# Kernel tuning notes

Measured on AMD Instinct MI355X. Metric: run time of the kernel, lower is better.

The kernel has to match this reference:

```python
import jax, jax.numpy as jnp
import numpy as np

B, S, E = 2, 2048, 1024
H, KV, D = 16, 4, 64
GC = 128          # ve_gate_channels
EPS = 1.1920929e-07  # torch F.rms_norm default eps for fp32
NEG = -1e30


def setup_inputs() -> dict:
    key = jax.random.key(0)
    ks = jax.random.split(key, 8)
    x = jax.random.normal(ks[0], (B, S, E), jnp.float32)
    ve = jax.random.normal(ks[1], (B, S, KV * D), jnp.float32)
    half = D // 2
    inv_freq = 1.0 / (10000.0 ** (np.arange(half, dtype=np.float64) / half))
    ang = np.arange(S, dtype=np.float64)[:, None] * inv_freq[None, :]
    cos = jnp.asarray(np.cos(ang), jnp.float32)[:, None, :]  # [S,1,D/2]
    sin = jnp.asarray(np.sin(ang), jnp.float32)[:, None, :]
    sc = E ** -0.5
    Wq = jax.random.normal(ks[2], (E, H * D), jnp.float32) * sc
    Wk = jax.random.normal(ks[3], (E, KV * D), jnp.float32) * sc
    Wv = jax.random.normal(ks[4], (E, KV * D), jnp.float32) * sc
    Wproj = jax.random.normal(ks[5], (E, E), jnp.float32) * sc
    Wgate = jax.random.normal(ks[6], (GC, KV), jnp.float32) * (GC ** -0.5)
    return {"x": x, "ve": ve, "cos": cos, "sin": sin, "Wq": Wq, "Wk": Wk,
            "Wv": Wv, "Wproj": Wproj, "Wgate": Wgate,
            "window_left": 1024, "window_right": 0}


def _rms(x):
    return x * jax.lax.rsqrt(jnp.mean(x * x, axis=-1, keepdims=True) + EPS)


def _rope(x, cos, sin):
    d = x.shape[-1] // 2
    x1, x2 = x[..., :d], x[..., d:]
    return jnp.concatenate([x1 * cos + x2 * sin, -x1 * sin + x2 * cos], axis=-1)


def reference(x, ve, cos, sin, Wq, Wk, Wv, Wproj, Wgate, window_left, window_right):
    b, s, e = x.shape
    q = (x @ Wq).reshape(b, s, H, D)
    k = (x @ Wk).reshape(b, s, KV, D)
    v = (x @ Wv).reshape(b, s, KV, D)
    # value-embedding gate: 2*sigmoid over first GC channels, per kv-head
    gate = 2.0 * jax.nn.sigmoid(x[..., :GC] @ Wgate)          # [B,S,KV]
    v = v + gate[..., None] * ve.reshape(b, s, KV, D)
    q = _rms(_rope(q, cos, sin))
    k = _rms(_rope(k, cos, sin))
    # GQA: repeat kv heads to match query heads
    g = H // KV
    kk = jnp.repeat(k, g, axis=2)                             # [B,S,H,D]
    vv = jnp.repeat(v, g, axis=2)
    scores = jnp.einsum('bihd,bjhd->bhij', q, kk) * (D ** -0.5)
    i = jnp.arange(s)[:, None]
    j = jnp.arange(s)[None, :]
    mask = (j <= i + window_right) & (j >= i - window_left) & (j <= i)
    scores = jnp.where(mask, scores, NEG)
    p = jax.nn.softmax(scores, axis=-1)
    y = jnp.einsum('bhij,bjhd->bihd', p, vv).reshape(b, s, H * D)
    return y @ Wproj
```

## Files before the change

kernel.cpp:

```cpp
#include <hip/hip_runtime.h>

typedef __bf16 bf16;
typedef __bf16 bf16x4 __attribute__((ext_vector_type(4)));
typedef __bf16 bf16x8 __attribute__((ext_vector_type(8)));
typedef float floatx4 __attribute__((ext_vector_type(4)));

#define EPS 1.1920929e-07f
#define QSCALE (0.125f * 1.44269504088896f)
#define SHIFT_C 11.5416f

__device__ __forceinline__ floatx4 mfma16(bf16x8 a, bf16x8 b, floatx4 c) {
  return __builtin_amdgcn_mfma_f32_16x16x32_bf16(a, b, c, 0, 0, 0);
}

__device__ __forceinline__ void gload16(const void* g, void* l) {
  __builtin_amdgcn_global_load_lds((const __attribute__((address_space(1))) unsigned int*)g,
                                   (__attribute__((address_space(3))) unsigned int*)l, 16, 0, 0);
}

__global__ void cast_gate_kernel(const float* __restrict__ x, const float* __restrict__ wgate,
                                 bf16* __restrict__ xb, float* __restrict__ gate) {
  int t = blockIdx.x, tid = threadIdx.x;
  const float* xr = x + (size_t)t * 1024;
  float4 v = *(const float4*)(xr + tid * 4);
  bf16x4 o = {(bf16)v.x, (bf16)v.y, (bf16)v.z, (bf16)v.w};
  *(bf16x4*)(xb + (size_t)t * 1024 + tid * 4) = o;
  if (tid < 64) {
    int c = (tid & 31) * 4;
#pragma unroll
    for (int kv = 0; kv < 4; kv++) {
      float g = v.x * wgate[(c + 0) * 4 + kv] + v.y * wgate[(c + 1) * 4 + kv] +
                v.z * wgate[(c + 2) * 4 + kv] + v.w * wgate[(c + 3) * 4 + kv];
      g += __shfl_xor(g, 1, 64);
      g += __shfl_xor(g, 2, 64);
      g += __shfl_xor(g, 4, 64);
      g += __shfl_xor(g, 8, 64);
      g += __shfl_xor(g, 16, 64);
      if (tid == 0) {
        int b = t >> 11, s = t & 2047;
        gate[((size_t)b * 4 + kv) * 2048 + s] = 2.f / (1.f + __expf(-g));
      }
    }
  }
}

__global__ void pack_w_kernel(const float* __restrict__ Wq, const float* __restrict__ Wk,
                              const float* __restrict__ Wv, const float* __restrict__ Wproj,
                              bf16* __restrict__ out_qkv, bf16* __restrict__ out_proj) {
  __shared__ float tile[32][33];
  int k0 = blockIdx.y * 32;
  int tx = threadIdx.x & 31, ty = threadIdx.x >> 5;
  if (blockIdx.x < 48) {
    int n0 = blockIdx.x * 32;
#pragma unroll
    for (int i = 0; i < 4; i++) {
      int k = k0 + ty + i * 8, n = n0 + tx;
      float v;
      if (n < 1024)      v = Wq[(size_t)k * 1024 + n];
      else if (n < 1280) v = Wk[(size_t)k * 256 + (n - 1024)];
      else               v = Wv[(size_t)k * 256 + (n - 1280)];
      tile[ty + i * 8][tx] = v;
    }
    __syncthreads();
#pragma unroll
    for (int i = 0; i < 4; i++) {
      int n = n0 + ty + i * 8, k = k0 + tx;
      out_qkv[(size_t)n * 1024 + k] = (bf16)tile[tx][ty + i * 8];
    }
  } else {
    int n0 = (blockIdx.x - 48) * 32;
#pragma unroll
    for (int i = 0; i < 4; i++)
      tile[ty + i * 8][tx] = Wproj[(size_t)(k0 + ty + i * 8) * 1024 + n0 + tx];
    __syncthreads();
#pragma unroll
    for (int i = 0; i < 4; i++)
      out_proj[(size_t)(n0 + ty + i * 8) * 1024 + k0 + tx] = (bf16)tile[tx][ty + i * 8];
  }
}

__global__ __launch_bounds__(256) void qkv_gemm_kernel(const bf16* __restrict__ A,
                                                       const bf16* __restrict__ Bt,
                                                       const float* __restrict__ ve,
                                                       const float* __restrict__ cosb,
                                                       const float* __restrict__ sinb,
                                                       const float* __restrict__ gate,
                                                       bf16* __restrict__ Qb,
                                                       bf16* __restrict__ Kf,
                                                       bf16* __restrict__ Vf) {
  __shared__ __align__(16) char smem[24576];
  bf16* As = (bf16*)smem;
  bf16* Bs = (bf16*)(smem + 16384);
  bf16* Ep = (bf16*)smem;
  const int K = 1024;
  const int tid = threadIdx.x;
  const int tile = blockIdx.x;
  const int m0 = blockIdx.y * 128, n0 = tile * 64;
  const int w = tid >> 6, lane = tid & 63;
  const int q = lane >> 4, r0 = lane & 15;
  const int lrow = lane >> 2, lcol = (lane & 3) * 8;
  const int b = m0 >> 11, s0 = m0 & 2047;

  floatx4 acc[2][4];
#pragma unroll
  for (int i = 0; i < 2; i++)
#pragma unroll
    for (int j = 0; j < 4; j++) acc[i][j] = (floatx4){0.f, 0.f, 0.f, 0.f};

  for (int k0 = 0; k0 < K; k0 += 64) {
    __syncthreads();
#pragma unroll
    for (int i = 0; i < 4; i++) {
      int g = w * 4 + i, s = g >> 3, rb = g & 7;
      gload16(A + (size_t)(m0 + rb * 16 + lrow) * K + k0 + s * 32 + lcol, &As[s * 4096 + rb * 512]);
    }
#pragma unroll
    for (int i = 0; i < 2; i++) {
      int g = w * 2 + i, s = g >> 2, rb = g & 3;
      gload16(Bt + (size_t)(n0 + rb * 16 + lrow) * K + k0 + s * 32 + lcol, &Bs[s * 2048 + rb * 512]);
    }
    __syncthreads();
#pragma unroll
    for (int s = 0; s < 2; s++) {
      bf16x8 af[2], bfr[4];
#pragma unroll
      for (int mt = 0; mt < 2; mt++) af[mt] = *(const bf16x8*)&As[s * 4096 + (w * 32 + mt * 16 + r0) * 32 + q * 8];
#pragma unroll
      for (int nt = 0; nt < 4; nt++) bfr[nt] = *(const bf16x8*)&Bs[s * 2048 + (nt * 16 + r0) * 32 + q * 8];
#pragma unroll
      for (int mt = 0; mt < 2; mt++)
#pragma unroll
        for (int nt = 0; nt < 4; nt++)
          acc[mt][nt] = mfma16(af[mt], bfr[nt], acc[mt][nt]);
    }
  }
  __syncthreads();

  if (tile < 16) {
    const int h = tile;
#pragma unroll
    for (int mt = 0; mt < 2; mt++) {
      float rvv[4][4];
#pragma unroll
      for (int ntp = 0; ntp < 2; ntp++) {
        int d31 = ntp * 16 + r0;
#pragma unroll
        for (int r = 0; r < 4; r++) {
          int s = s0 + w * 32 + mt * 16 + q * 4 + r;
          float c = cosb[s * 32 + d31], sn = sinb[s * 32 + d31];
          float v1 = acc[mt][ntp][r], v2 = acc[mt][ntp + 2][r];
          rvv[ntp][r] = v1 * c + v2 * sn;
          rvv[ntp + 2][r] = v2 * c - v1 * sn;
        }
      }
#pragma unroll
      for (int r = 0; r < 4; r++) {
        float ss = 0.f;
#pragma unroll
        for (int nt = 0; nt < 4; nt++) ss += rvv[nt][r] * rvv[nt][r];
        ss += __shfl_xor(ss, 1, 64);
        ss += __shfl_xor(ss, 2, 64);
        ss += __shfl_xor(ss, 4, 64);
        ss += __shfl_xor(ss, 8, 64);
        float sc = rsqrtf(ss * (1.f / 64.f) + EPS) * QSCALE;
        int row = w * 32 + mt * 16 + q * 4 + r;
#pragma unroll
        for (int nt = 0; nt < 4; nt++)
          Ep[row * 72 + nt * 16 + r0] = (bf16)(rvv[nt][r] * sc);
      }
    }
    __syncthreads();
#pragma unroll
    for (int p = 0; p < 4; p++) {
      int g = p * 256 + tid;
      int row = g >> 3, chunk = g & 7;
      *(uint4*)&Qb[(((size_t)b * 16 + h) * 2048 + s0 + row) * 64 + chunk * 8] =
          *(const uint4*)&Ep[row * 72 + chunk * 8];
    }
  } else if (tile < 20) {
    const int kv = tile - 16;
#pragma unroll
    for (int mt = 0; mt < 2; mt++) {
      float rvv[4][4];
#pragma unroll
      for (int ntp = 0; ntp < 2; ntp++) {
        int d31 = ntp * 16 + r0;
#pragma unroll
        for (int r = 0; r < 4; r++) {
          int s = s0 + w * 32 + mt * 16 + q * 4 + r;
          float c = cosb[s * 32 + d31], sn = sinb[s * 32 + d31];
          float v1 = acc[mt][ntp][r], v2 = acc[mt][ntp + 2][r];
          rvv[ntp][r] = v1 * c + v2 * sn;
          rvv[ntp + 2][r] = v2 * c - v1 * sn;
        }
      }
#pragma unroll
      for (int r = 0; r < 4; r++) {
        float ss = 0.f;
#pragma unroll
        for (int nt = 0; nt < 4; nt++) ss += rvv[nt][r] * rvv[nt][r];
        ss += __shfl_xor(ss, 1, 64);
        ss += __shfl_xor(ss, 2, 64);
        ss += __shfl_xor(ss, 4, 64);
        ss += __shfl_xor(ss, 8, 64);
        float sc = rsqrtf(ss * (1.f / 64.f) + EPS);
        int row = w * 32 + mt * 16 + q * 4 + r;
#pragma unroll
        for (int nt = 0; nt < 4; nt++)
          Ep[row * 72 + nt * 16 + r0] = (bf16)(rvv[nt][r] * sc);
      }
    }
    __syncthreads();
    {
      int tk = (s0 >> 5) + w;
      size_t tb = ((size_t)(b * 4 + kv) * 64 + tk) * 2048;
#pragma unroll
      for (int u = 0; u < 4; u++) {
        int joff = (u >= 2) ? 16 : 0, doff = (u & 1) * 32;
        bf16x8 f = *(const bf16x8*)&Ep[(w * 32 + joff + r0) * 72 + doff + q * 8];
        *(bf16x8*)&Kf[tb + u * 512 + lane * 8] = f;
      }
    }
  } else {
    const int kv = tile - 20;
    const float* gbase = gate + ((size_t)b * 4 + kv) * 2048;
#pragma unroll
    for (int mt = 0; mt < 2; mt++) {
#pragma unroll
      for (int r = 0; r < 4; r++) {
        int row = w * 32 + mt * 16 + q * 4 + r;
        float gg = gbase[s0 + row];
#pragma unroll
        for (int nt = 0; nt < 4; nt++) {
          int d = nt * 16 + r0;
          float vv = acc[mt][nt][r] + gg * ve[(size_t)(m0 + row) * 256 + kv * 64 + d];
          Ep[row * 72 + d] = (bf16)vv;
        }
      }
    }
    __syncthreads();
    {
      int tk = (s0 >> 5) + w;
      size_t tb = ((size_t)(b * 4 + kv) * 64 + tk) * 2048;
#pragma unroll
      for (int nt = 0; nt < 4; nt++) {
        bf16 tmp[8];
#pragma unroll
        for (int e = 0; e < 8; e++) {
          int jl = w * 32 + (e >> 2) * 16 + 4 * q + (e & 3);
          tmp[e] = Ep[jl * 72 + nt * 16 + r0];
        }
        *(uint4*)&Vf[tb + nt * 512 + lane * 8] = *(uint4*)tmp;
      }
    }
  }
}

__global__ __launch_bounds__(256) void proj_gemm_kernel(const bf16* __restrict__ A,
                                                        const bf16* __restrict__ Bt,
                                                        float* __restrict__ Cout) {
  __shared__ __align__(16) bf16 As[2 * 128 * 32];
  __shared__ __align__(16) bf16 Bs[2 * 64 * 32];
  const int K = 1024, N = 1024;
  const int tid = threadIdx.x;
  const int m0 = blockIdx.y * 128, n0 = blockIdx.x * 64;
  const int w = tid >> 6, lane = tid & 63;
  const int q = lane >> 4, r0 = lane & 15;
  const int lrow = lane >> 2, lcol = (lane & 3) * 8;

  floatx4 acc[2][4];
#pragma unroll
  for (int i = 0; i < 2; i++)
#pragma unroll
    for (int j = 0; j < 4; j++) acc[i][j] = (floatx4){0.f, 0.f, 0.f, 0.f};

  for (int k0 = 0; k0 < K; k0 += 64) {
    __syncthreads();
#pragma unroll
    for (int i = 0; i < 4; i++) {
      int g = w * 4 + i, s = g >> 3, rb = g & 7;
      gload16(A + (size_t)(m0 + rb * 16 + lrow) * K + k0 + s * 32 + lcol, &As[s * 4096 + rb * 512]);
    }
#pragma unroll
    for (int i = 0; i < 2; i++) {
      int g = w * 2 + i, s = g >> 2, rb = g & 3;
      gload16(Bt + (size_t)(n0 + rb * 16 + lrow) * K + k0 + s * 32 + lcol, &Bs[s * 2048 + rb * 512]);
    }
    __syncthreads();
#pragma unroll
    for (int s = 0; s < 2; s++) {
      bf16x8 af[2], bfr[4];
#pragma unroll
      for (int mt = 0; mt < 2; mt++) af[mt] = *(const bf16x8*)&As[s * 4096 + (w * 32 + mt * 16 + r0) * 32 + q * 8];
#pragma unroll
      for (int nt = 0; nt < 4; nt++) bfr[nt] = *(const bf16x8*)&Bs[s * 2048 + (nt * 16 + r0) * 32 + q * 8];
#pragma unroll
      for (int mt = 0; mt < 2; mt++)
#pragma unroll
        for (int nt = 0; nt < 4; nt++)
          acc[mt][nt] = mfma16(af[mt], bfr[nt], acc[mt][nt]);
    }
  }
#pragma unroll
  for (int mt = 0; mt < 2; mt++)
#pragma unroll
    for (int nt = 0; nt < 4; nt++)
#pragma unroll
      for (int r = 0; r < 4; r++) {
        int row = m0 + w * 32 + mt * 16 + q * 4 + r;
        int col = n0 + nt * 16 + r0;
        Cout[(size_t)row * N + col] = acc[mt][nt][r];
      }
}

__global__ __launch_bounds__(512) void attn_kernel(const bf16* __restrict__ Qb,
                                                   const bf16* __restrict__ Kf,
                                                   const bf16* __restrict__ Vf,
                                                   const int* __restrict__ wlp,
                                                   const int* __restrict__ wrp,
                                                   bf16* __restrict__ Yb) {
  const int wl = wlp[0];
  const int wrc = min(wrp[0], 0);
  const int blk = blockIdx.x;
  const int cpair = blk & 31, bkv = blk >> 5;
  const int b = bkv >> 2, kvh = bkv & 3;
  const int w = threadIdx.x >> 6, lane = threadIdx.x & 63;
  const int q = lane >> 4, r0 = lane & 15;
  const int h = kvh * 4 + (w & 3);
  const int cm = (w < 4) ? cpair : 63 - cpair;
  const int q0 = cm * 32;
  const int qA = q0, qB = q0 + 16;

  const bf16* qbase = Qb + (((size_t)b * 16 + h) * 2048 + qA + r0) * 64;
  bf16x8 aqA0 = *(const bf16x8*)(qbase + q * 8);
  bf16x8 aqA1 = *(const bf16x8*)(qbase + 32 + q * 8);
  bf16x8 aqB0 = *(const bf16x8*)(qbase + 16 * 64 + q * 8);
  bf16x8 aqB1 = *(const bf16x8*)(qbase + 16 * 64 + 32 + q * 8);

  floatx4 OA[4], OB[4];
#pragma unroll
  for (int nt = 0; nt < 4; nt++) {
    OA[nt] = (floatx4){0.f, 0.f, 0.f, 0.f};
    OB[nt] = (floatx4){0.f, 0.f, 0.f, 0.f};
  }
  floatx4 LA = (floatx4){0.f, 0.f, 0.f, 0.f};
  floatx4 LB = LA;

  const bf16 onev = (bf16)1.0f;
  const bf16x8 ones = {onev, onev, onev, onev, onev, onev, onev, onev};

  const int jlo = max(0, q0 - wl) & ~31;
  const int jhi = q0 + 31 + wrc;
  const int count = ((jhi - jlo) >> 5) + 1;
  const int tile0 = jlo >> 5;

  const bf16* kfb = Kf + ((size_t)(b * 4 + kvh) * 64) * 2048 + lane * 8;
  const bf16* vfb = Vf + ((size_t)(b * 4 + kvh) * 64) * 2048 + lane * 8;

  bf16x8 kf[4], vf[4], nk[4], nv[4];
#pragma unroll
  for (int u = 0; u < 4; u++) {
    kf[u] = *(const bf16x8*)(kfb + (size_t)tile0 * 2048 + u * 512);
    vf[u] = *(const bf16x8*)(vfb + (size_t)tile0 * 2048 + u * 512);
  }

  for (int t = 0; t < count; t++) {
    const int j0 = jlo + (t << 5);
    const int tn = (t + 1 < count) ? tile0 + t + 1 : tile0 + t;
#pragma unroll
    for (int u = 0; u < 4; u++) {
      nk[u] = *(const bf16x8*)(kfb + (size_t)tn * 2048 + u * 512);
      nv[u] = *(const bf16x8*)(vfb + (size_t)tn * 2048 + u * 512);
    }

    floatx4 sA0 = (floatx4){-SHIFT_C, -SHIFT_C, -SHIFT_C, -SHIFT_C};
    floatx4 sA1 = sA0, sB0 = sA0, sB1 = sA0;
    sA0 = mfma16(kf[0], aqA0, sA0);
    sA0 = mfma16(kf[1], aqA1, sA0);
    sA1 = mfma16(kf[2], aqA0, sA1);
    sA1 = mfma16(kf[3], aqA1, sA1);
    sB0 = mfma16(kf[0], aqB0, sB0);
    sB0 = mfma16(kf[1], aqB1, sB0);
    sB1 = mfma16(kf[2], aqB0, sB1);
    sB1 = mfma16(kf[3], aqB1, sB1);

    bf16x8 paA, paB;
    if (j0 >= qA + 15 - wl && j0 + 31 <= qA + wrc) {
#pragma unroll
      for (int r = 0; r < 4; r++) {
        paA[r] = (bf16)exp2f(sA0[r]);
        paA[4 + r] = (bf16)exp2f(sA1[r]);
      }
    } else {
      const int i = qA + r0;
#pragma unroll
      for (int r = 0; r < 4; r++) {
        int ja = j0 + 4 * q + r, jb = ja + 16;
        bool va = (ja <= i + wrc) && (ja >= i - wl);
        bool vb = (jb <= i + wrc) && (jb >= i - wl);
        paA[r] = va ? (bf16)exp2f(sA0[r]) : (bf16)0.f;
        paA[4 + r] = vb ? (bf16)exp2f(sA1[r]) : (bf16)0.f;
      }
    }
    if (j0 >= qB + 15 - wl && j0 + 31 <= qB + wrc) {
#pragma unroll
      for (int r = 0; r < 4; r++) {
        paB[r] = (bf16)exp2f(sB0[r]);
        paB[4 + r] = (bf16)exp2f(sB1[r]);
      }
    } else {
      const int i = qB + r0;
#pragma unroll
      for (int r = 0; r < 4; r++) {
        int ja = j0 + 4 * q + r, jb = ja + 16;
        bool va = (ja <= i + wrc) && (ja >= i - wl);
        bool vb = (jb <= i + wrc) && (jb >= i - wl);
        paB[r] = va ? (bf16)exp2f(sB0[r]) : (bf16)0.f;
        paB[4 + r] = vb ? (bf16)exp2f(sB1[r]) : (bf16)0.f;
      }
    }

    LA = mfma16(paA, ones, LA);
    LB = mfma16(paB, ones, LB);
#pragma unroll
    for (int nt = 0; nt < 4; nt++) {
      OA[nt] = mfma16(paA, vf[nt], OA[nt]);
      OB[nt] = mfma16(paB, vf[nt], OB[nt]);
    }

#pragma unroll
    for (int u = 0; u < 4; u++) { kf[u] = nk[u]; vf[u] = nv[u]; }
  }

  float invA[4], invB[4];
#pragma unroll
  for (int r = 0; r < 4; r++) {
    invA[r] = 1.f / LA[r];
    invB[r] = 1.f / LB[r];
  }
#pragma unroll
  for (int nt = 0; nt < 4; nt++)
#pragma unroll
    for (int r = 0; r < 4; r++) {
      int iA = qA + q * 4 + r;
      Yb[((size_t)b * 2048 + iA) * 1024 + h * 64 + nt * 16 + r0] = (bf16)(OA[nt][r] * invA[r]);
      int iB = qB + q * 4 + r;
      Yb[((size_t)b * 2048 + iB) * 1024 + h * 64 + nt * 16 + r0] = (bf16)(OB[nt][r] * invB[r]);
    }
}

extern "C" void kernel_launch(void* const* d_in, const int* in_sizes, int n_in,
                              void* d_out, int out_size, void* d_ws, size_t ws_size,
                              hipStream_t stream) {
  const float* x     = (const float*)d_in[0];
  const float* ve    = (const float*)d_in[1];
  const float* cosb  = (const float*)d_in[2];
  const float* sinb  = (const float*)d_in[3];
  const float* Wq    = (const float*)d_in[4];
  const float* Wk    = (const float*)d_in[5];
  const float* Wv    = (const float*)d_in[6];
  const float* Wproj = (const float*)d_in[7];
  const float* Wgate = (const float*)d_in[8];
  const int* wl      = (const int*)d_in[9];
  const int* wr      = (const int*)d_in[10];

  char* ws = (char*)d_ws;
  bf16* Xb      = (bf16*)(ws);
  bf16* Wqkv_t  = (bf16*)(ws + 8388608);
  bf16* Wproj_t = (bf16*)(ws + 11534336);
  bf16* Qb      = (bf16*)(ws + 13631488);
  bf16* Kf      = (bf16*)(ws + 22020096);
  bf16* Vf      = (bf16*)(ws + 24117248);
  bf16* Yb      = (bf16*)(ws + 26214400);
  float* gateb  = (float*)(ws + 34603008);

  cast_gate_kernel<<<4096, 256, 0, stream>>>(x, Wgate, Xb, gateb);
  pack_w_kernel<<<dim3(80, 32), 256, 0, stream>>>(Wq, Wk, Wv, Wproj, Wqkv_t, Wproj_t);
  qkv_gemm_kernel<<<dim3(24, 32), 256, 0, stream>>>(Xb, Wqkv_t, ve, cosb, sinb, gateb, Qb, Kf, Vf);
  attn_kernel<<<256, 512, 0, stream>>>(Qb, Kf, Vf, wl, wr, Yb);
  proj_gemm_kernel<<<dim3(16, 32), 256, 0, stream>>>(Yb, Wproj_t, (float*)d_out);
}
```

Baseline: 171.4 us.

## Merge prep kernels and split attention into smaller 16-row blocks

Merges the x cast/gate kernel and the weight pack/transpose kernel into one launch, removing one kernel launch and its tail. Restructures attention so each 256-thread block handles one 16-query-row chunk for four heads, launching 1024 blocks ordered heaviest-first instead of 256 blocks that paired mirrored 32-row chunks. It also adds s_setprio around the MFMA groups. This raises the number of blocks and occupancy for load balance, but K/V tiles are now reloaded per 16 query rows instead of shared across two 16-row halves, which increases K/V memory traffic.

```diff
diff --git a/kernel.cpp b/kernel.cpp
--- a/kernel.cpp
+++ b/kernel.cpp
@@ -18,64 +18,69 @@
                                    (__attribute__((address_space(3))) unsigned int*)l, 16, 0, 0);
 }
 
-__global__ void cast_gate_kernel(const float* __restrict__ x, const float* __restrict__ wgate,
-                                 bf16* __restrict__ xb, float* __restrict__ gate) {
-  int t = blockIdx.x, tid = threadIdx.x;
-  const float* xr = x + (size_t)t * 1024;
-  float4 v = *(const float4*)(xr + tid * 4);
-  bf16x4 o = {(bf16)v.x, (bf16)v.y, (bf16)v.z, (bf16)v.w};
-  *(bf16x4*)(xb + (size_t)t * 1024 + tid * 4) = o;
-  if (tid < 64) {
-    int c = (tid & 31) * 4;
-#pragma unroll
-    for (int kv = 0; kv < 4; kv++) {
-      float g = v.x * wgate[(c + 0) * 4 + kv] + v.y * wgate[(c + 1) * 4 + kv] +
-                v.z * wgate[(c + 2) * 4 + kv] + v.w * wgate[(c + 3) * 4 + kv];
-      g += __shfl_xor(g, 1, 64);
-      g += __shfl_xor(g, 2, 64);
-      g += __shfl_xor(g, 4, 64);
-      g += __shfl_xor(g, 8, 64);
-      g += __shfl_xor(g, 16, 64);
-      if (tid == 0) {
-        int b = t >> 11, s = t & 2047;
-        gate[((size_t)b * 4 + kv) * 2048 + s] = 2.f / (1.f + __expf(-g));
-      }
-    }
-  }
-}
-
-__global__ void pack_w_kernel(const float* __restrict__ Wq, const float* __restrict__ Wk,
-                              const float* __restrict__ Wv, const float* __restrict__ Wproj,
-                              bf16* __restrict__ out_qkv, bf16* __restrict__ out_proj) {
+__global__ void prep_kernel(const float* __restrict__ x, const float* __restrict__ wgate,
+                            const float* __restrict__ Wq, const float* __restrict__ Wk,
+                            const float* __restrict__ Wv, const float* __restrict__ Wproj,
+                            bf16* __restrict__ xb, float* __restrict__ gate,
+                            bf16* __restrict__ out_qkv, bf16* __restrict__ out_proj) {
   __shared__ float tile[32][33];
-  int k0 = blockIdx.y * 32;
-  int tx = threadIdx.x & 31, ty = threadIdx.x >> 5;
-  if (blockIdx.x < 48) {
-    int n0 = blockIdx.x * 32;
-#pragma unroll
-    for (int i = 0; i < 4; i++) {
-      int k = k0 + ty + i * 8, n = n0 + tx;
-      float v;
-      if (n < 1024)      v = Wq[(size_t)k * 1024 + n];
-      else if (n < 1280) v = Wk[(size_t)k * 256 + (n - 1024)];
-      else               v = Wv[(size_t)k * 256 + (n - 1280)];
-      tile[ty + i * 8][tx] = v;
-    }
-    __syncthreads();
-#pragma unroll
-    for (int i = 0; i < 4; i++) {
-      int n = n0 + ty + i * 8, k = k0 + tx;
-      out_qkv[(size_t)n * 1024 + k] = (bf16)tile[tx][ty + i * 8];
+  const int tid = threadIdx.x;
+  if (blockIdx.x < 4096) {
+    int t = blockIdx.x;
+    const float* xr = x + (size_t)t * 1024;
+    float4 v = *(const float4*)(xr + tid * 4);
+    bf16x4 o = {(bf16)v.x, (bf16)v.y, (bf16)v.z, (bf16)v.w};
+    *(bf16x4*)(xb + (size_t)t * 1024 + tid * 4) = o;
+    if (tid < 64) {
+      int c = (tid & 31) * 4;
+#pragma unroll
+      for (int kv = 0; kv < 4; kv++) {
+        float g = v.x * wgate[(c + 0) * 4 + kv] + v.y * wgate[(c + 1) * 4 + kv] +
+                  v.z * wgate[(c + 2) * 4 + kv] + v.w * wgate[(c + 3) * 4 + kv];
+        g += __shfl_xor(g, 1, 64);
+        g += __shfl_xor(g, 2, 64);
+        g += __shfl_xor(g, 4, 64);
+        g += __shfl_xor(g, 8, 64);
+        g += __shfl_xor(g, 16, 64);
+        if (tid == 0) {
+          int b = t >> 11, s = t & 2047;
+          gate[((size_t)b * 4 + kv) * 2048 + s] = 2.f / (1.f + __expf(-g));
+        }
+      }
     }
   } else {
-    int n0 = (blockIdx.x - 48) * 32;
-#pragma unroll
-    for (int i = 0; i < 4; i++)
-      tile[ty + i * 8][tx] = Wproj[(size_t)(k0 + ty + i * 8) * 1024 + n0 + tx];
-    __syncthreads();
-#pragma unroll
-    for (int i = 0; i < 4; i++)
-      out_proj[(size_t)(n0 + ty + i * 8) * 1024 + k0 + tx] = (bf16)tile[tx][ty + i * 8];
+    int j = blockIdx.x - 4096;
+    int ky = j / 80;
+    int nx = j - ky * 80;
+    int k0 = ky * 32;
+    int tx = tid & 31, ty = tid >> 5;
+    if (nx < 48) {
+      int n0 = nx * 32;
+#pragma unroll
+      for (int i = 0; i < 4; i++) {
+        int k = k0 + ty + i * 8, n = n0 + tx;
+        float v;
+        if (n < 1024)      v = Wq[(size_t)k * 1024 + n];
+        else if (n < 1280) v = Wk[(size_t)k * 256 + (n - 1024)];
+        else               v = Wv[(size_t)k * 256 + (n - 1280)];
+        tile[ty + i * 8][tx] = v;
+      }
+      __syncthreads();
+#pragma unroll
+      for (int i = 0; i < 4; i++) {
+        int n = n0 + ty + i * 8, k = k0 + tx;
+        out_qkv[(size_t)n * 1024 + k] = (bf16)tile[tx][ty + i * 8];
+      }
+    } else {
+      int n0 = (nx - 48) * 32;
+#pragma unroll
+      for (int i = 0; i < 4; i++)
+        tile[ty + i * 8][tx] = Wproj[(size_t)(k0 + ty + i * 8) * 1024 + n0 + tx];
+      __syncthreads();
+#pragma unroll
+      for (int i = 0; i < 4; i++)
+        out_proj[(size_t)(n0 + ty + i * 8) * 1024 + k0 + tx] = (bf16)tile[tx][ty + i * 8];
+    }
   }
 }
 
@@ -313,44 +318,37 @@
       }
 }
 
-__global__ __launch_bounds__(512) void attn_kernel(const bf16* __restrict__ Qb,
-                                                   const bf16* __restrict__ Kf,
-                                                   const bf16* __restrict__ Vf,
-                                                   const int* __restrict__ wlp,
-                                                   const int* __restrict__ wrp,
-                                                   bf16* __restrict__ Yb) {
+__global__ __launch_bounds__(256, 4) void attn_kernel(const bf16* __restrict__ Qb,
+                                                      const bf16* __restrict__ Kf,
+                                                      const bf16* __restrict__ Vf,
+                                                      const int* __restrict__ wlp,
+                                                      const int* __restrict__ wrp,
+                                                      bf16* __restrict__ Yb) {
   const int wl = wlp[0];
   const int wrc = min(wrp[0], 0);
   const int blk = blockIdx.x;
-  const int cpair = blk & 31, bkv = blk >> 5;
+  const int bkv = blk & 7;
   const int b = bkv >> 2, kvh = bkv & 3;
+  const int cm = 127 - (blk >> 3);
   const int w = threadIdx.x >> 6, lane = threadIdx.x & 63;
   const int q = lane >> 4, r0 = lane & 15;
-  const int h = kvh * 4 + (w & 3);
-  const int cm = (w < 4) ? cpair : 63 - cpair;
-  const int q0 = cm * 32;
-  const int qA = q0, qB = q0 + 16;
-
-  const bf16* qbase = Qb + (((size_t)b * 16 + h) * 2048 + qA + r0) * 64;
-  bf16x8 aqA0 = *(const bf16x8*)(qbase + q * 8);
-  bf16x8 aqA1 = *(const bf16x8*)(qbase + 32 + q * 8);
-  bf16x8 aqB0 = *(const bf16x8*)(qbase + 16 * 64 + q * 8);
-  bf16x8 aqB1 = *(const bf16x8*)(qbase + 16 * 64 + 32 + q * 8);
-
-  floatx4 OA[4], OB[4];
-#pragma unroll
-  for (int nt = 0; nt < 4; nt++) {
-    OA[nt] = (floatx4){0.f, 0.f, 0.f, 0.f};
-    OB[nt] = (floatx4){0.f, 0.f, 0.f, 0.f};
-  }
-  floatx4 LA = (floatx4){0.f, 0.f, 0.f, 0.f};
-  floatx4 LB = LA;
+  const int h = kvh * 4 + w;
+  const int q0 = cm << 4;
+
+  const bf16* qbase = Qb + (((size_t)b * 16 + h) * 2048 + q0 + r0) * 64;
+  bf16x8 aq0 = *(const bf16x8*)(qbase + q * 8);
+  bf16x8 aq1 = *(const bf16x8*)(qbase + 32 + q * 8);
+
+  floatx4 O[4];
+#pragma unroll
+  for (int nt = 0; nt < 4; nt++) O[nt] = (floatx4){0.f, 0.f, 0.f, 0.f};
+  floatx4 L = (floatx4){0.f, 0.f, 0.f, 0.f};
 
   const bf16 onev = (bf16)1.0f;
   const bf16x8 ones = {onev, onev, onev, onev, onev, onev, onev, onev};
 
   const int jlo = max(0, q0 - wl) & ~31;
-  const int jhi = q0 + 31 + wrc;
+  const int jhi = q0 + 15 + wrc;
   const int count = ((jhi - jlo) >> 5) + 1;
   const int tile0 = jlo >> 5;
 
@@ -373,79 +371,53 @@
       nv[u] = *(const bf16x8*)(vfb + (size_t)tn * 2048 + u * 512);
     }
 
-    floatx4 sA0 = (floatx4){-SHIFT_C, -SHIFT_C, -SHIFT_C, -SHIFT_C};
-    floatx4 sA1 = sA0, sB0 = sA0, sB1 = sA0;
-    sA0 = mfma16(kf[0], aqA0, sA0);
-    sA0 = mfma16(kf[1], aqA1, sA0);
-    sA1 = mfma16(kf[2], aqA0, sA1);
-    sA1 = mfma16(kf[3], aqA1, sA1);
-    sB0 = mfma16(kf[0], aqB0, sB0);
-    sB0 = mfma16(kf[1], aqB1, sB0);
-    sB1 = mfma16(kf[2], aqB0, sB1);
-    sB1 = mfma16(kf[3], aqB1, sB1);
-
-    bf16x8 paA, paB;
-    if (j0 >= qA + 15 - wl && j0 + 31 <= qA + wrc) {
-#pragma unroll
-      for (int r = 0; r < 4; r++) {
-        paA[r] = (bf16)exp2f(sA0[r]);
-        paA[4 + r] = (bf16)exp2f(sA1[r]);
+    floatx4 s0 = (floatx4){-SHIFT_C, -SHIFT_C, -SHIFT_C, -SHIFT_C};
+    floatx4 s1 = s0;
+    __builtin_amdgcn_s_setprio(1);
+    s0 = mfma16(kf[0], aq0, s0);
+    s0 = mfma16(kf[1], aq1, s0);
+    s1 = mfma16(kf[2], aq0, s1);
+    s1 = mfma16(kf[3], aq1, s1);
+    __builtin_amdgcn_s_setprio(0);
+
+    bf16x8 pa;
+    if (j0 >= q0 + 15 - wl && j0 + 31 <= q0 + wrc) {
+#pragma unroll
+      for (int r = 0; r < 4; r++) {
+        pa[r] = (bf16)exp2f(s0[r]);
+        pa[4 + r] = (bf16)exp2f(s1[r]);
       }
     } else {
-      const int i = qA + r0;
+      const int i = q0 + r0;
 #pragma unroll
       for (int r = 0; r < 4; r++) {
         int ja = j0 + 4 * q + r, jb = ja + 16;
         bool va = (ja <= i + wrc) && (ja >= i - wl);
         bool vb = (jb <= i + wrc) && (jb >= i - wl);
-        paA[r] = va ? (bf16)exp2f(sA0[r]) : (bf16)0.f;
-        paA[4 + r] = vb ? (bf16)exp2f(sA1[r]) : (bf16)0.f;
-      }
-    }
-    if (j0 >= qB + 15 - wl && j0 + 31 <= qB + wrc) {
-#pragma unroll
-      for (int r = 0; r < 4; r++) {
-        paB[r] = (bf16)exp2f(sB0[r]);
-        paB[4 + r] = (bf16)exp2f(sB1[r]);
-      }
-    } else {
-      const int i = qB + r0;
-#pragma unroll
-      for (int r = 0; r < 4; r++) {
-        int ja = j0 + 4 * q + r, jb = ja + 16;
-        bool va = (ja <= i + wrc) && (ja >= i - wl);
-        bool vb = (jb <= i + wrc) && (jb >= i - wl);
-        paB[r] = va ? (bf16)exp2f(sB0[r]) : (bf16)0.f;
-        paB[4 + r] = vb ? (bf16)exp2f(sB1[r]) : (bf16)0.f;
-      }
-    }
-
-    LA = mfma16(paA, ones, LA);
-    LB = mfma16(paB, ones, LB);
-#pragma unroll
-    for (int nt = 0; nt < 4; nt++) {
-      OA[nt] = mfma16(paA, vf[nt], OA[nt]);
-      OB[nt] = mfma16(paB, vf[nt], OB[nt]);
-    }
+        pa[r] = va ? (bf16)exp2f(s0[r]) : (bf16)0.f;
+        pa[4 + r] = vb ? (bf16)exp2f(s1[r]) : (bf16)0.f;
+      }
+    }
+
+    __builtin_amdgcn_s_setprio(1);
+    L = mfma16(pa, ones, L);
+#pragma unroll
+    for (int nt = 0; nt < 4; nt++) O[nt] = mfma16(pa, vf[nt], O[nt]);
+    __builtin_amdgcn_s_setprio(0);
 
 #pragma unroll
     for (int u = 0; u < 4; u++) { kf[u] = nk[u]; vf[u] = nv[u]; }
   }
 
-  float invA[4], invB[4];
-#pragma unroll
-  for (int r = 0; r < 4; r++) {
-    invA[r] = 1.f / LA[r];
-    invB[r] = 1.f / LB[r];
-  }
+  float inv[4];
+#pragma unroll
+  for (int r = 0; r < 4; r++) inv[r] = 1.f / L[r];
 #pragma unroll
   for (int nt = 0; nt < 4; nt++)
 #pragma unroll
     for (int r = 0; r < 4; r++) {
-      int iA = qA + q * 4 + r;
-      Yb[((size_t)b * 2048 + iA) * 1024 + h * 64 + nt * 16 + r0] = (bf16)(OA[nt][r] * invA[r]);
-      int iB = qB + q * 4 + r;
-      Yb[((size_t)b * 2048 + iB) * 1024 + h * 64 + nt * 16 + r0] = (bf16)(OB[nt][r] * invB[r]);
+      int i = q0 + q * 4 + r;
+      Yb[((size_t)b * 2048 + i) * 1024 + h * 64 + nt * 16 + r0] = (bf16)(O[nt][r] * inv[r]);
     }
 }
 
@@ -474,9 +446,8 @@
   bf16* Yb      = (bf16*)(ws + 26214400);
   float* gateb  = (float*)(ws + 34603008);
 
-  cast_gate_kernel<<<4096, 256, 0, stream>>>(x, Wgate, Xb, gateb);
-  pack_w_kernel<<<dim3(80, 32), 256, 0, stream>>>(Wq, Wk, Wv, Wproj, Wqkv_t, Wproj_t);
+  prep_kernel<<<4096 + 2560, 256, 0, stream>>>(x, Wgate, Wq, Wk, Wv, Wproj, Xb, gateb, Wqkv_t, Wproj_t);
   qkv_gemm_kernel<<<dim3(24, 32), 256, 0, stream>>>(Xb, Wqkv_t, ve, cosb, sinb, gateb, Qb, Kf, Vf);
-  attn_kernel<<<256, 512, 0, stream>>>(Qb, Kf, Vf, wl, wr, Yb);
+  attn_kernel<<<1024, 256, 0, stream>>>(Qb, Kf, Vf, wl, wr, Yb);
   proj_gemm_kernel<<<dim3(16, 32), 256, 0, stream>>>(Yb, Wproj_t, (float*)d_out);
 }
```

After: 167.3 us. -2.4%, faster.
